# Kernel tuning notes

Hardware: AMD Instinct MI355X
Metric: run time of the kernel (lower is better)

## Reference

```python
import jax, jax.numpy as jnp
import numpy as np

N_NODES = 10000
N_EDGES = 320000
N_PAIRS = 8192
IN_CH = 128
HIDDEN = 256
OUT_CH = 1


def setup_inputs() -> dict:
    key = jax.random.key(0)
    k1, k2, k3, k4, k5 = jax.random.split(key, 5)
    x = jax.random.normal(k1, (N_NODES, IN_CH), dtype=jnp.float32)
    edge_index = jax.random.randint(k2, (2, N_EDGES), 0, N_NODES, dtype=jnp.int64)
    tar_ei = jax.random.randint(k3, (2, N_PAIRS), 0, N_NODES, dtype=jnp.int64)
    # xsmlp params (Linear(2*in, hidden) -> ReLU -> Linear(hidden, out))
    W1 = jax.random.normal(k4, (HIDDEN, 2 * IN_CH), dtype=jnp.float32) * (1.0 / np.sqrt(2 * IN_CH))
    b1 = jnp.zeros((HIDDEN,), dtype=jnp.float32)
    W2 = jax.random.normal(k5, (OUT_CH, HIDDEN), dtype=jnp.float32) * (1.0 / np.sqrt(HIDDEN))
    b2 = jnp.zeros((OUT_CH,), dtype=jnp.float32)
    return {"x": x, "edge_index": edge_index, "tar_ei": tar_ei,
            "W1": W1, "b1": b1, "W2": W2, "b2": b2}


def reference(x, edge_index, tar_ei, W1, b1, W2, b2):
    # k=2 path of NCNPredictor.
    N = x.shape[0]
    # Symmetric binary adjacency (coalesce + fill_value_(1.0) => values all 1).
    A = (jnp.zeros((N, N), dtype=x.dtype)
         .at[edge_index[0], edge_index[1]].set(1.0)
         .at[edge_index[1], edge_index[0]].set(1.0))
    i, j = tar_ei[0], tar_ei[1]
    # xij: elementwise product of endpoint features  [B, d]
    xij = x[i] * x[j]
    # Common-neighbor indicator rows: cn_1_1 = adj1[tar_i] * adj1[tar_j]  [B, N]
    cn = A[i] * A[j]
    # spmm_add(cn_1_1, x): sum features of common neighbors  [B, d]
    cn_emb = cn @ x
    xs = jnp.concatenate([xij, cn_emb], axis=-1)  # [B, 2d]
    # xs.relu() in the original is not in-place -> no-op, faithfully omitted.
    h = jax.nn.relu(xs @ W1.T + b1)
    return h @ W2.T + b2
```

## Files before the change

kernel.cpp:

```cpp
#include <hip/hip_runtime.h>

#define N_NODES 10000
#define N_EDGES 320000
#define N_PAIRS 8192
#define IN_CH   128
#define HIDDEN  256
#define K_DIM   256
#define WPR     320
#define WPR4    (WPR / 4)
#define TILE_B  16
#define CN_CAP  64
#define ZERO_BLOCKS (N_NODES * WPR / 4 / 256)
#define PACK_BLOCKS 32
#define ADJ_BLOCKS  (N_EDGES / 256)

typedef __attribute__((ext_vector_type(8))) short  short8;
typedef __attribute__((ext_vector_type(4))) float  f32x4;

static __device__ inline short f2bf(float f) {
    union { float f; unsigned u; } c; c.f = f;
    unsigned r = (c.u + 0x7FFFu + ((c.u >> 16) & 1u)) >> 16;
    return (short)r;
}

__global__ __launch_bounds__(256) void zero_pack_kernel(uint4* __restrict__ adj4,
                                                        const float* __restrict__ W1,
                                                        short* __restrict__ W1B) {
    int bid = blockIdx.x;
    int tid = threadIdx.x;
    if (bid < ZERO_BLOCKS) {
        adj4[(size_t)bid * 256 + tid] = make_uint4(0u, 0u, 0u, 0u);
    } else {
        int t2 = (bid - ZERO_BLOCKS) * 256 + tid;
        int ks = t2 >> 10;
        int t  = (t2 >> 6) & 15;
        int l  = t2 & 63;
        int n  = t * 16 + (l & 15);
        int kb = ks * 32 + ((l >> 4) << 3);
        const float* src = W1 + (size_t)n * K_DIM + kb;
        short* dst = W1B + ((size_t)(ks * 16 + t) * 64 + l) * 8;
#pragma unroll
        for (int e = 0; e < 8; ++e) dst[e] = f2bf(src[e]);
    }
}

__global__ __launch_bounds__(256) void build_adj_kernel(const int* __restrict__ ei,
                                                        unsigned int* __restrict__ adj) {
    int e = blockIdx.x * blockDim.x + threadIdx.x;
    int u = ei[e];
    int v = ei[N_EDGES + e];
    atomicOr(&adj[(size_t)u * WPR + (v >> 5)], 1u << (v & 31));
    atomicOr(&adj[(size_t)v * WPR + (u >> 5)], 1u << (u & 31));
}

__global__ __launch_bounds__(512) void fused_kernel(const float* __restrict__ x,
                                                    const int* __restrict__ tei,
                                                    const unsigned int* __restrict__ adj,
                                                    const short* __restrict__ W1B,
                                                    const float* __restrict__ b1,
                                                    const float* __restrict__ W2,
                                                    const float* __restrict__ b2,
                                                    float* __restrict__ out) {
    __shared__ float4 s_xs4[TILE_B * 64];
    __shared__ int    s_ij[TILE_B][2];
    __shared__ int    s_cnt[TILE_B];
    __shared__ int    s_cnl[TILE_B][CN_CAP];
    __shared__ float  s_part[TILE_B][8];

    const int tid = threadIdx.x;
    const int p0 = blockIdx.x * TILE_B;

    if (tid < TILE_B) {
        s_ij[tid][0] = tei[p0 + tid];
        s_ij[tid][1] = tei[N_PAIRS + p0 + tid];
        s_cnt[tid] = 0;
    }
    {
        int zb = tid >> 5, zu = 32 + (tid & 31);
        s_xs4[zb * 64 + zu] = make_float4(0.f, 0.f, 0.f, 0.f);
    }
    __syncthreads();

    const int b = tid >> 5;
    const int s = tid & 31;
    const int i = s_ij[b][0];
    const int j = s_ij[b][1];

    const float4* xi4 = (const float4*)(x + (size_t)i * IN_CH);
    const float4* xj4 = (const float4*)(x + (size_t)j * IN_CH);
    float4 va = xi4[s];
    float4 vb = xj4[s];

    const uint4* ri4 = (const uint4*)(adj + (size_t)i * WPR);
    const uint4* rj4 = (const uint4*)(adj + (size_t)j * WPR);
    for (int q = s; q < WPR4; q += 32) {
        uint4 a = ri4[q];
        uint4 c = rj4[q];
        unsigned int m[4] = { a.x & c.x, a.y & c.y, a.z & c.z, a.w & c.w };
#pragma unroll
        for (int ww = 0; ww < 4; ++ww) {
            unsigned int mm = m[ww];
            while (mm) {
                int bit = __builtin_ctz(mm);
                mm &= mm - 1;
                int n = q * 128 + ww * 32 + bit;
                int pos = atomicAdd(&s_cnt[b], 1);
                if (pos < CN_CAP) {
                    s_cnl[b][pos] = n;
                } else {
                    const float* xn = x + (size_t)n * IN_CH;
                    for (int d = 0; d < IN_CH; ++d) {
                        int u = 32 + (d >> 2);
                        float* base = (float*)&s_xs4[b * 64 + (u ^ (b & 7))];
                        atomicAdd(&base[d & 3], xn[d]);
                    }
                }
            }
        }
    }

    s_xs4[b * 64 + (s ^ (b & 7))] =
        make_float4(va.x * vb.x, va.y * vb.y, va.z * vb.z, va.w * vb.w);

    {
        int cnt = s_cnt[b];
        if (cnt > CN_CAP) cnt = CN_CAP;
        int u = (32 + s) ^ (b & 7);
        float4 d0 = s_xs4[b * 64 + u];
        for (int c = 0; c < cnt; ++c) {
            const float4* xn4 = (const float4*)(x + (size_t)s_cnl[b][c] * IN_CH);
            float4 v = xn4[s];
            d0 = make_float4(d0.x + v.x, d0.y + v.y, d0.z + v.z, d0.w + v.w);
        }
        s_xs4[b * 64 + u] = d0;
    }
    __syncthreads();

    const int w    = tid >> 6;
    const int lane = tid & 63;
    const int t0 = w * 2, t1 = w * 2 + 1;
    const int mr = lane & 15;
    const int kb = lane >> 4;

    f32x4 acc0 = {0.f, 0.f, 0.f, 0.f};
    f32x4 acc1 = {0.f, 0.f, 0.f, 0.f};

    const short8* W1B8 = (const short8*)W1B;
#pragma unroll
    for (int ks = 0; ks < 8; ++ks) {
        int f0 = ks * 8 + kb * 2;
        float4 x0 = s_xs4[mr * 64 + (f0 ^ (mr & 7))];
        float4 x1 = s_xs4[mr * 64 + ((f0 + 1) ^ (mr & 7))];
        short8 af;
        af[0] = f2bf(x0.x); af[1] = f2bf(x0.y); af[2] = f2bf(x0.z); af[3] = f2bf(x0.w);
        af[4] = f2bf(x1.x); af[5] = f2bf(x1.y); af[6] = f2bf(x1.z); af[7] = f2bf(x1.w);
        int fb = (ks * 16 + t0) * 64 + lane;
        short8 bf0 = W1B8[fb];
        short8 bf1 = W1B8[fb + 64];
        acc0 = __builtin_amdgcn_mfma_f32_16x16x32_bf16(af, bf0, acc0, 0, 0, 0);
        acc1 = __builtin_amdgcn_mfma_f32_16x16x32_bf16(af, bf1, acc1, 0, 0, 0);
    }

    const int ncol = lane & 15;
    const float b10 = b1[t0 * 16 + ncol];
    const float b11 = b1[t1 * 16 + ncol];
    const float w20 = W2[t0 * 16 + ncol];
    const float w21 = W2[t1 * 16 + ncol];

    float sum[4];
#pragma unroll
    for (int r = 0; r < 4; ++r)
        sum[r] = w20 * fmaxf(acc0[r] + b10, 0.f) + w21 * fmaxf(acc1[r] + b11, 0.f);

#pragma unroll
    for (int r = 0; r < 4; ++r) {
        float v = sum[r];
        v += __shfl_xor(v, 1);
        v += __shfl_xor(v, 2);
        v += __shfl_xor(v, 4);
        v += __shfl_xor(v, 8);
        if ((lane & 15) == 0) s_part[kb * 4 + r][w] = v;
    }
    __syncthreads();

    if (tid < TILE_B) {
        float r = b2[0];
#pragma unroll
        for (int ww = 0; ww < 8; ++ww) r += s_part[tid][ww];
        out[p0 + tid] = r;
    }
}

extern "C" void kernel_launch(void* const* d_in, const int* in_sizes, int n_in,
                              void* d_out, int out_size, void* d_ws, size_t ws_size,
                              hipStream_t stream) {
    const float* x   = (const float*)d_in[0];
    const int*   ei  = (const int*)d_in[1];
    const int*   tei = (const int*)d_in[2];
    const float* W1  = (const float*)d_in[3];
    const float* b1  = (const float*)d_in[4];
    const float* W2  = (const float*)d_in[5];
    const float* b2  = (const float*)d_in[6];
    float* out = (float*)d_out;

    unsigned char* ws = (unsigned char*)d_ws;
    const size_t adj_bytes = (size_t)N_NODES * WPR * sizeof(unsigned int);
    unsigned int* adj = (unsigned int*)ws;
    short* W1B = (short*)(ws + adj_bytes);

    zero_pack_kernel<<<ZERO_BLOCKS + PACK_BLOCKS, 256, 0, stream>>>((uint4*)adj, W1, W1B);
    build_adj_kernel<<<ADJ_BLOCKS, 256, 0, stream>>>(ei, adj);
    fused_kernel<<<N_PAIRS / TILE_B, 512, 0, stream>>>(x, tei, adj, W1B, b1, W2, b2, out);
}
```

Baseline: 55.94 us.

## Double threads per pair in fused kernel and split common-neighbor gather

```diff
diff --git a/kernel.cpp b/kernel.cpp
--- a/kernel.cpp
+++ b/kernel.cpp
@@ -9,7 +9,7 @@
 #define WPR     320
 #define WPR4    (WPR / 4)
 #define TILE_B  16
-#define CN_CAP  64
+#define CN_CAP  128
 #define ZERO_BLOCKS (N_NODES * WPR / 4 / 256)
 #define PACK_BLOCKS 32
 #define ADJ_BLOCKS  (N_EDGES / 256)
@@ -53,19 +53,19 @@
     atomicOr(&adj[(size_t)v * WPR + (u >> 5)], 1u << (u & 31));
 }
 
-__global__ __launch_bounds__(512) void fused_kernel(const float* __restrict__ x,
-                                                    const int* __restrict__ tei,
-                                                    const unsigned int* __restrict__ adj,
-                                                    const short* __restrict__ W1B,
-                                                    const float* __restrict__ b1,
-                                                    const float* __restrict__ W2,
-                                                    const float* __restrict__ b2,
-                                                    float* __restrict__ out) {
+__global__ __launch_bounds__(1024, 8) void fused_kernel(const float* __restrict__ x,
+                                                        const int* __restrict__ tei,
+                                                        const unsigned int* __restrict__ adj,
+                                                        const short* __restrict__ W1B,
+                                                        const float* __restrict__ b1,
+                                                        const float* __restrict__ W2,
+                                                        const float* __restrict__ b2,
+                                                        float* __restrict__ out) {
     __shared__ float4 s_xs4[TILE_B * 64];
     __shared__ int    s_ij[TILE_B][2];
     __shared__ int    s_cnt[TILE_B];
     __shared__ int    s_cnl[TILE_B][CN_CAP];
-    __shared__ float  s_part[TILE_B][8];
+    __shared__ float  s_part[TILE_B][16];
 
     const int tid = threadIdx.x;
     const int p0 = blockIdx.x * TILE_B;
@@ -75,25 +75,26 @@
         s_ij[tid][1] = tei[N_PAIRS + p0 + tid];
         s_cnt[tid] = 0;
     }
-    {
+    if (tid < TILE_B * 32) {
         int zb = tid >> 5, zu = 32 + (tid & 31);
         s_xs4[zb * 64 + zu] = make_float4(0.f, 0.f, 0.f, 0.f);
     }
     __syncthreads();
 
-    const int b = tid >> 5;
-    const int s = tid & 31;
+    const int b = tid >> 6;
+    const int s = tid & 63;
     const int i = s_ij[b][0];
     const int j = s_ij[b][1];
 
-    const float4* xi4 = (const float4*)(x + (size_t)i * IN_CH);
-    const float4* xj4 = (const float4*)(x + (size_t)j * IN_CH);
-    float4 va = xi4[s];
-    float4 vb = xj4[s];
+    float4 va, vb;
+    if (s < 32) {
+        va = ((const float4*)(x + (size_t)i * IN_CH))[s];
+        vb = ((const float4*)(x + (size_t)j * IN_CH))[s];
+    }
 
     const uint4* ri4 = (const uint4*)(adj + (size_t)i * WPR);
     const uint4* rj4 = (const uint4*)(adj + (size_t)j * WPR);
-    for (int q = s; q < WPR4; q += 32) {
+    for (int q = s; q < WPR4; q += 64) {
         uint4 a = ri4[q];
         uint4 c = rj4[q];
         unsigned int m[4] = { a.x & c.x, a.y & c.y, a.z & c.z, a.w & c.w };
@@ -119,31 +120,51 @@
         }
     }
 
-    s_xs4[b * 64 + (s ^ (b & 7))] =
-        make_float4(va.x * vb.x, va.y * vb.y, va.z * vb.z, va.w * vb.w);
+    if (s < 32) {
+        s_xs4[b * 64 + (s ^ (b & 7))] =
+            make_float4(va.x * vb.x, va.y * vb.y, va.z * vb.z, va.w * vb.w);
+    }
 
     {
         int cnt = s_cnt[b];
         if (cnt > CN_CAP) cnt = CN_CAP;
-        int u = (32 + s) ^ (b & 7);
-        float4 d0 = s_xs4[b * 64 + u];
-        for (int c = 0; c < cnt; ++c) {
-            const float4* xn4 = (const float4*)(x + (size_t)s_cnl[b][c] * IN_CH);
-            float4 v = xn4[s];
-            d0 = make_float4(d0.x + v.x, d0.y + v.y, d0.z + v.z, d0.w + v.w);
-        }
-        s_xs4[b * 64 + u] = d0;
+        const int half = s >> 5;
+        const int su = s & 31;
+        float4 dA = make_float4(0.f, 0.f, 0.f, 0.f);
+        float4 dB = make_float4(0.f, 0.f, 0.f, 0.f);
+        int c = half;
+        for (; c + 2 < cnt; c += 4) {
+            const float4* qa = (const float4*)(x + (size_t)s_cnl[b][c]     * IN_CH);
+            const float4* qb = (const float4*)(x + (size_t)s_cnl[b][c + 2] * IN_CH);
+            float4 v0 = qa[su], v1 = qb[su];
+            dA = make_float4(dA.x + v0.x, dA.y + v0.y, dA.z + v0.z, dA.w + v0.w);
+            dB = make_float4(dB.x + v1.x, dB.y + v1.y, dB.z + v1.z, dB.w + v1.w);
+        }
+        if (c < cnt) {
+            const float4* qa = (const float4*)(x + (size_t)s_cnl[b][c] * IN_CH);
+            float4 v0 = qa[su];
+            dA = make_float4(dA.x + v0.x, dA.y + v0.y, dA.z + v0.z, dA.w + v0.w);
+        }
+        dA = make_float4(dA.x + dB.x, dA.y + dB.y, dA.z + dB.z, dA.w + dB.w);
+        float ox = __shfl_xor(dA.x, 32);
+        float oy = __shfl_xor(dA.y, 32);
+        float oz = __shfl_xor(dA.z, 32);
+        float ow = __shfl_xor(dA.w, 32);
+        if (s < 32) {
+            int u = (32 + su) ^ (b & 7);
+            float4 base = s_xs4[b * 64 + u];
+            s_xs4[b * 64 + u] = make_float4(base.x + dA.x + ox, base.y + dA.y + oy,
+                                            base.z + dA.z + oz, base.w + dA.w + ow);
+        }
     }
     __syncthreads();
 
     const int w    = tid >> 6;
     const int lane = tid & 63;
-    const int t0 = w * 2, t1 = w * 2 + 1;
     const int mr = lane & 15;
     const int kb = lane >> 4;
 
-    f32x4 acc0 = {0.f, 0.f, 0.f, 0.f};
-    f32x4 acc1 = {0.f, 0.f, 0.f, 0.f};
+    f32x4 acc = {0.f, 0.f, 0.f, 0.f};
 
     const short8* W1B8 = (const short8*)W1B;
 #pragma unroll
@@ -154,27 +175,17 @@
         short8 af;
         af[0] = f2bf(x0.x); af[1] = f2bf(x0.y); af[2] = f2bf(x0.z); af[3] = f2bf(x0.w);
         af[4] = f2bf(x1.x); af[5] = f2bf(x1.y); af[6] = f2bf(x1.z); af[7] = f2bf(x1.w);
-        int fb = (ks * 16 + t0) * 64 + lane;
-        short8 bf0 = W1B8[fb];
-        short8 bf1 = W1B8[fb + 64];
-        acc0 = __builtin_amdgcn_mfma_f32_16x16x32_bf16(af, bf0, acc0, 0, 0, 0);
-        acc1 = __builtin_amdgcn_mfma_f32_16x16x32_bf16(af, bf1, acc1, 0, 0, 0);
+        short8 bf = W1B8[(ks * 16 + w) * 64 + lane];
+        acc = __builtin_amdgcn_mfma_f32_16x16x32_bf16(af, bf, acc, 0, 0, 0);
     }
 
     const int ncol = lane & 15;
-    const float b10 = b1[t0 * 16 + ncol];
-    const float b11 = b1[t1 * 16 + ncol];
-    const float w20 = W2[t0 * 16 + ncol];
-    const float w21 = W2[t1 * 16 + ncol];
-
-    float sum[4];
-#pragma unroll
-    for (int r = 0; r < 4; ++r)
-        sum[r] = w20 * fmaxf(acc0[r] + b10, 0.f) + w21 * fmaxf(acc1[r] + b11, 0.f);
+    const float b1v = b1[w * 16 + ncol];
+    const float w2v = W2[w * 16 + ncol];
 
 #pragma unroll
     for (int r = 0; r < 4; ++r) {
-        float v = sum[r];
+        float v = w2v * fmaxf(acc[r] + b1v, 0.f);
         v += __shfl_xor(v, 1);
         v += __shfl_xor(v, 2);
         v += __shfl_xor(v, 4);
@@ -186,7 +197,7 @@
     if (tid < TILE_B) {
         float r = b2[0];
 #pragma unroll
-        for (int ww = 0; ww < 8; ++ww) r += s_part[tid][ww];
+        for (int ww = 0; ww < 16; ++ww) r += s_part[tid][ww];
         out[p0 + tid] = r;
     }
 }
@@ -210,5 +221,5 @@
 
     zero_pack_kernel<<<ZERO_BLOCKS + PACK_BLOCKS, 256, 0, stream>>>((uint4*)adj, W1, W1B);
     build_adj_kernel<<<ADJ_BLOCKS, 256, 0, stream>>>(ei, adj);
-    fused_kernel<<<N_PAIRS / TILE_B, 512, 0, stream>>>(x, tei, adj, W1B, b1, W2, b2, out);
-}
+    fused_kernel<<<N_PAIRS / TILE_B, 1024, 0, stream>>>(x, tei, adj, W1B, b1, W2, b2, out);
+}
```

Measured after the change: 56.37 us. No clear change (+0.8%).
